# Kernel tuning notes

Hardware: AMD Instinct MI355X
Metric: run time of the kernel (lower is better)

The kernel has to match this reference:

```python
import jax, jax.numpy as jnp
import numpy as np

KERNEL_MUL = 2.0
KERNEL_NUM = 5
THRESH = 0.5            # cfg.FIXED_CONFIDENCE_THRESHOLD
LAMBDA = 1.0            # cfg.ECDA_CLASS_ATTENTION_LAMBDA
GAMMA = 0.1             # cfg.ECDA_COMPACTNESS_WEIGHT_GAMMA
DELTA = 0.01            # cfg.ECDA_REPULSION_WEIGHT_DELTA
NUM_CLASSES = 8
N, D = 2048, 256


def _sqdist(a, b):
    # pairwise squared euclidean distances [Na, Nb]
    d2 = (jnp.sum(a * a, 1)[:, None] + jnp.sum(b * b, 1)[None, :]
          - 2.0 * (a @ b.T))
    return jnp.maximum(d2, 0.0)


def setup_inputs() -> dict:
    key = jax.random.key(0)
    ks = jax.random.split(key, 6)
    return {
        'clean_feats': jax.random.normal(ks[0], (N, D), dtype=jnp.float32),
        'noisy_feats': jax.random.normal(ks[1], (N, D), dtype=jnp.float32),
        'clean_labels': jax.random.randint(ks[2], (N,), 0, NUM_CLASSES),
        'noisy_labels': jax.random.randint(ks[3], (N,), 0, NUM_CLASSES),
        'noisy_mask': jax.random.uniform(ks[4], (N,), dtype=jnp.float32),
        'noisy_scores': jax.random.uniform(ks[5], (N,), dtype=jnp.float32),
        'class_weights_wce': jax.random.uniform(jax.random.fold_in(key, 7), (NUM_CLASSES,), dtype=jnp.float32),
    }


def reference(clean_feats, noisy_feats, clean_labels, noisy_labels,
              noisy_mask, noisy_scores, class_weights_wce):
    C = class_weights_wce.shape[0]
    mask_n = noisy_mask > THRESH                       # float mask -> bool (cfg threshold)

    # full pairwise squared-distance matrices, reused by every class
    D_cc = _sqdist(clean_feats, clean_feats)           # [Nc, Nc]
    D_nn = _sqdist(noisy_feats, noisy_feats)           # [Nn, Nn]
    D_cn = _sqdist(clean_feats, noisy_feats)           # [Nc, Nn]

    classes = jnp.arange(C)
    Ms = (clean_labels[None, :] == classes[:, None]).astype(jnp.float32)   # [C, Nc]
    Mn = ((noisy_labels[None, :] == classes[:, None]) & mask_n[None, :]).astype(jnp.float32)  # [C, Nn]

    # noisy centroids + repulsion over valid classes (torch.pdist mean, negated)
    counts_n = Mn.sum(1)
    centroids = (Mn @ noisy_feats) / jnp.maximum(counts_n, 1.0)[:, None]
    valid = counts_n > 0
    Dcen = jnp.sqrt(jnp.maximum(_sqdist(centroids, centroids), 1e-12))
    pair = jnp.triu(jnp.ones((C, C), bool), 1) & valid[:, None] & valid[None, :]
    npairs = pair.sum().astype(jnp.float32)
    repulsion = jnp.where(valid.sum() > 1,
                          -jnp.sum(jnp.where(pair, Dcen, 0.0)) / jnp.maximum(npairs, 1.0),
                          0.0)

    attn = jnp.exp(LAMBDA * (class_weights_wce.mean() - class_weights_wce))
    half = KERNEL_MUL ** (KERNEL_NUM // 2)

    total = jnp.float32(0.0)
    for c in range(C):
        ms = Ms[c]                                     # clean weights (ones, masked)
        mn = Mn[c]
        n_s, n_t = ms.sum(), mn.sum()
        n = n_s + n_t
        # bandwidth from subset L2 sum (detached, as in .data)
        sumL2 = ms @ (D_cc @ ms) + mn @ (D_nn @ mn) + 2.0 * (ms @ (D_cn @ mn))
        sumL2 = jax.lax.stop_gradient(sumL2)
        bw0 = sumL2 / jnp.maximum(n * n - n, 1.0) / half
        wn = noisy_scores * mn                          # masked noisy weights
        ss = tt = st = jnp.float32(0.0)
        for k in range(KERNEL_NUM):
            bw = bw0 * (KERNEL_MUL ** k) + 1e-8
            ss = ss + ms @ (jnp.exp(-D_cc / bw) @ ms)
            tt = tt + wn @ (jnp.exp(-D_nn / bw) @ wn)
            st = st + ms @ (jnp.exp(-D_cn / bw) @ wn)
        sw = wn.sum()
        term_ss = ss / (n_s * n_s + 1e-8)
        term_tt = tt / (sw * sw + 1e-8)
        term_st = st / (n_s * sw + 1e-8)
        mmd = term_ss + term_tt - 2.0 * term_st
        compact = jnp.sum(mn * jnp.sum((noisy_feats - centroids[c]) ** 2, 1)) / jnp.maximum(n_t, 1.0)
        loss_c = mmd + GAMMA * compact + DELTA * repulsion
        total = total + jnp.where((n_s >= 2) & (n_t >= 2), attn[c] * loss_c, 0.0)
    return total
```

## Files before the change

kernel.cpp:

```cpp
#include <hip/hip_runtime.h>
#include <math.h>


static constexpr int NC = 8;
static constexpr int NN = 2048;
static constexpr int DD = 256;

static constexpr int OFF_CNT_S = 0;
static constexpr int OFF_CNT_T = 64;
static constexpr int OFF_SW    = 128;
static constexpr int OFF_COEF  = 192;
static constexpr int OFF_CCOMP = 256;
static constexpr int OFF_SQSP  = 1024;
static constexpr int OFF_SQTP  = 1536;
static constexpr int OFF_HDR   = 2048;
static constexpr int OFF_VSP   = 4096;
static constexpr int OFF_VTP   = 135168;
static constexpr int OFF_VS    = 266240;
static constexpr int OFF_VT    = 274432;
static constexpr int OFF_QBFS  = 282624;
static constexpr int OFF_QBFT  = 348160;
static constexpr int OFF_WTP   = 413696;
static constexpr size_t OFF_PKS = 479232;
static constexpr size_t OFF_PKT = 8867840;

typedef __attribute__((ext_vector_type(8))) short bf16x8;
typedef __attribute__((ext_vector_type(4))) float f32x4;

__device__ inline float wred64(float v) {
  for (int o = 32; o > 0; o >>= 1) v += __shfl_xor(v, o, 64);
  return v;
}
__device__ inline float brs256(float v, float* sh4) {
  for (int o = 32; o > 0; o >>= 1) v += __shfl_xor(v, o, 64);
  int w = threadIdx.x >> 6, ln = threadIdx.x & 63;
  __syncthreads();
  if (ln == 0) sh4[w] = v;
  __syncthreads();
  float r = 0.f;
  if (threadIdx.x == 0) r = sh4[0] + sh4[1] + sh4[2] + sh4[3];
  return r;
}

__global__ __launch_bounds__(256) void ecda_pack(
    const float* __restrict__ cfeat, const float* __restrict__ nfeat,
    const int* __restrict__ clab, const int* __restrict__ nlab,
    const float* __restrict__ nmask, const float* __restrict__ nscore,
    char* __restrict__ ws, float* __restrict__ out) {
  __shared__ int   ls_idx[NN];
  __shared__ float ls_wt[NN];
  __shared__ int   ls_cntw[4];
  __shared__ float ls_mom[4][256];
  __shared__ float ls_sq[4];
  __shared__ float sh4[4];
  int tid = threadIdx.x, bx = blockIdx.x;
  int wv = tid >> 6, lane = tid & 63;
  int typ = bx >> 7, c = (bx >> 4) & 7, chunk = bx & 15;

  if (bx == 0 && tid == 0) out[0] = 0.f;

  const int* labs = typ ? nlab : clab;
  const float* feats = typ ? nfeat : cfeat;

  int rb = wv * 512;
  int lv[8]; float mv[8], sv[8];
#pragma unroll
  for (int it = 0; it < 8; ++it) {
    int i = rb + it * 64 + lane;
    lv[it] = labs[i];
    if (typ) { mv[it] = nmask[i]; sv[it] = nscore[i]; }
  }
  unsigned long long msks[8];
  int cntw = 0;
#pragma unroll
  for (int it = 0; it < 8; ++it) {
    bool m = (lv[it] == c) && (!typ || mv[it] > 0.5f);
    msks[it] = __ballot(m);
    cntw += __popcll(msks[it]);
  }
  if (lane == 0) ls_cntw[wv] = cntw;
  __syncthreads();
  int base = 0;
  for (int w2 = 0; w2 < wv; ++w2) base += ls_cntw[w2];
#pragma unroll
  for (int it = 0; it < 8; ++it) {
    bool m = (msks[it] >> lane) & 1ull;
    int pos = __popcll(msks[it] & ((1ull << lane) - 1ull));
    if (m) {
      ls_idx[base + pos] = rb + it * 64 + lane;
      ls_wt[base + pos] = typ ? sv[it] : 1.f;
    }
    base += __popcll(msks[it]);
  }
  __syncthreads();
  int count = ls_cntw[0] + ls_cntw[1] + ls_cntw[2] + ls_cntw[3];

  if (chunk == 0) {
    if (tid == 0) (typ ? (int*)(ws + OFF_CNT_T) : (int*)(ws + OFF_CNT_S))[c] = count;
    if (typ) {
      float s = 0.f;
      for (int i = tid; i < count; i += 256) s += ls_wt[i];
      s = brs256(s, sh4);
      if (tid == 0) ((float*)(ws + OFF_SW))[c] = s;
    }
  }

  unsigned short* pk = (unsigned short*)(ws + (typ ? OFF_PKT : OFF_PKS)) + (size_t)c * NN * DD;
  float* qarr = (float*)(ws + (typ ? OFF_QBFT : OFF_QBFS)) + c * NN;
  float* wtp  = (float*)(ws + OFF_WTP) + c * NN;
  float vax = 0.f, vay = 0.f, vaz = 0.f, vaw = 0.f, qlane = 0.f;
  int mstart = chunk * 4 + wv;
  for (int m0 = mstart; m0 < count; m0 += 256) {
    int mm[4]; bool act[4]; float4 v[4];
#pragma unroll
    for (int b = 0; b < 4; ++b) {
      int m = m0 + b * 64;
      act[b] = (m < count);
      mm[b] = act[b] ? m : m0;
    }
#pragma unroll
    for (int b = 0; b < 4; ++b) {
      int idx = ls_idx[mm[b]];
      v[b] = *(const float4*)&feats[(size_t)idx * DD + lane * 4];
    }
#pragma unroll
    for (int b = 0; b < 4; ++b) {
      unsigned ux = __float_as_uint(v[b].x); ux = (ux + 0x7fffu + ((ux >> 16) & 1u)) & 0xffff0000u;
      unsigned uy = __float_as_uint(v[b].y); uy = (uy + 0x7fffu + ((uy >> 16) & 1u)) & 0xffff0000u;
      unsigned uz = __float_as_uint(v[b].z); uz = (uz + 0x7fffu + ((uz >> 16) & 1u)) & 0xffff0000u;
      unsigned uw = __float_as_uint(v[b].w); uw = (uw + 0x7fffu + ((uw >> 16) & 1u)) & 0xffff0000u;
      float rx = __uint_as_float(ux), ry = __uint_as_float(uy);
      float rz = __uint_as_float(uz), rw = __uint_as_float(uw);
      float rq = wred64(rx * rx + ry * ry + rz * rz + rw * rw);
      if (act[b]) {
        vax += v[b].x; vay += v[b].y; vaz += v[b].z; vaw += v[b].w;
        qlane += v[b].x * v[b].x + v[b].y * v[b].y + v[b].z * v[b].z + v[b].w * v[b].w;
        ushort4 b4;
        b4.x = (unsigned short)(ux >> 16); b4.y = (unsigned short)(uy >> 16);
        b4.z = (unsigned short)(uz >> 16); b4.w = (unsigned short)(uw >> 16);
        *(ushort4*)&pk[(size_t)mm[b] * DD + lane * 4] = b4;
        if (lane == 0) {
          qarr[mm[b]] = rq;
          if (typ) wtp[mm[b]] = ls_wt[mm[b]];
        }
      }
    }
  }
  float sqa = wred64(qlane);
  ls_mom[wv][lane * 4 + 0] = vax; ls_mom[wv][lane * 4 + 1] = vay;
  ls_mom[wv][lane * 4 + 2] = vaz; ls_mom[wv][lane * 4 + 3] = vaw;
  if (lane == 0) ls_sq[wv] = sqa;
  __syncthreads();
  float s = ls_mom[0][tid] + ls_mom[1][tid] + ls_mom[2][tid] + ls_mom[3][tid];
  float* vp = (float*)(ws + (typ ? OFF_VTP : OFF_VSP)) + (c * 16 + chunk) * 256;
  vp[tid] = s;
  if (tid == 0)
    ((float*)(ws + (typ ? OFF_SQTP : OFF_SQSP)))[c * 16 + chunk] =
        ls_sq[0] + ls_sq[1] + ls_sq[2] + ls_sq[3];
}

__global__ __launch_bounds__(256) void ecda_scalars(
    const float* __restrict__ cw, char* __restrict__ ws) {
  __shared__ float sh4[4];
  int c = blockIdx.x, tid = threadIdx.x;
  const float* vsp = (const float*)(ws + OFF_VSP);
  const float* vtp = (const float*)(ws + OFF_VTP);
  float vsd = 0.f, vtd = 0.f;
#pragma unroll
  for (int ch = 0; ch < 16; ++ch) {
    vsd += vsp[(c * 16 + ch) * 256 + tid];
    vtd += vtp[(c * 16 + ch) * 256 + tid];
  }
  ((float*)(ws + OFF_VS))[c * 256 + tid] = vsd;
  ((float*)(ws + OFF_VT))[c * 256 + tid] = vtd;
  float dss = brs256(vsd * vsd, sh4);
  float dtt = brs256(vtd * vtd, sh4);
  float dst = brs256(vsd * vtd, sh4);
  if (tid == 0) {
    const float* sqsp = (const float*)(ws + OFF_SQSP);
    const float* sqtp = (const float*)(ws + OFF_SQTP);
    float sqs = 0.f, sqt = 0.f;
    for (int ch = 0; ch < 16; ++ch) { sqs += sqsp[c * 16 + ch]; sqt += sqtp[c * 16 + ch]; }
    int nsi = ((const int*)(ws + OFF_CNT_S))[c];
    int nti = ((const int*)(ws + OFF_CNT_T))[c];
    float ns = (float)nsi, nt = (float)nti, n = ns + nt;
    float sumL2 = 2.f * ns * sqs - 2.f * dss
                + 2.f * nt * sqt - 2.f * dtt
                + 2.f * (nt * sqs + ns * sqt - 2.f * dst);
    float bw0 = sumL2 / fmaxf(n * n - n, 1.f) * 0.25f;
    float ib[5];
    float mul = 1.f;
    for (int k = 0; k < 5; ++k) { ib[k] = 1.f / (bw0 * mul + 1e-8f); mul *= 2.f; }
    float meanw = 0.f;
    for (int c2 = 0; c2 < NC; ++c2) meanw += cw[c2];
    meanw *= (1.f / NC);
    float attn = expf(meanw - cw[c]);
    float coef = (nsi >= 2 && nti >= 2) ? attn : 0.f;
    float swc = ((const float*)(ws + OFF_SW))[c];
    float scc = coef / (ns * ns + 1e-8f);
    float snn = coef / (swc * swc + 1e-8f);
    float scn = -2.f * coef / (ns * swc + 1e-8f);
    float* hdr = (float*)(ws + OFF_HDR);
    for (int ty = 0; ty < 3; ++ty) {
      float* h = hdr + (ty * 8 + c) * 8;
      int na = (ty == 1) ? nti : nsi;
      int nb = (ty == 0) ? nsi : nti;
      h[0] = __int_as_float(na);
      h[1] = __int_as_float(nb);
      h[2] = (ty == 0) ? scc : (ty == 1) ? snn : scn;
      h[3] = ib[0]; h[4] = ib[1]; h[5] = ib[2]; h[6] = ib[3]; h[7] = ib[4];
    }
    float mx = fmaxf(nt, 1.f);
    float compact = (sqt - 2.f * dtt / mx + nt * dtt / (mx * mx)) / mx;
    ((float*)(ws + OFF_COEF))[c] = coef;
    ((float*)(ws + OFF_CCOMP))[c] = coef * 0.1f * compact;
  }
}

__global__ __launch_bounds__(256) void ecda_pairs(
    const float* __restrict__ cw, char* __restrict__ ws,
    float* __restrict__ out) {
  __shared__ float shred[4];
  __shared__ float dcen[28];
  int tid = threadIdx.x, bx = blockIdx.x;
  int wv = tid >> 6, lane = tid & 63;

  if (bx == 384) {
    const int* cnt_t = (const int*)(ws + OFF_CNT_T);
    const float* vt = (const float*)(ws + OFF_VT);
    for (int t = wv; t < 28; t += 4) {
      int a = 0, r = t;
      while (r >= 7 - a) { r -= 7 - a; ++a; }
      int b = a + 1 + r;
      float ima = 1.f / fmaxf((float)cnt_t[a], 1.f);
      float imb = 1.f / fmaxf((float)cnt_t[b], 1.f);
      float4 x = *(const float4*)&vt[a * DD + lane * 4];
      float4 y = *(const float4*)&vt[b * DD + lane * 4];
      float dx = x.x * ima - y.x * imb, dy = x.y * ima - y.y * imb;
      float dz = x.z * ima - y.z * imb, dw = x.w * ima - y.w * imb;
      float ssum = wred64(dx * dx + dy * dy + dz * dz + dw * dw);
      if (lane == 0) dcen[t] = sqrtf(fmaxf(ssum, 1e-12f));
    }
    __syncthreads();
    if (tid == 0) {
      int nvalid = 0;
      for (int c2 = 0; c2 < NC; ++c2) nvalid += (cnt_t[c2] > 0);
      float sumD = 0.f; int np = 0; int p = 0;
      for (int a = 0; a < NC; ++a)
        for (int b = a + 1; b < NC; ++b) {
          if (cnt_t[a] > 0 && cnt_t[b] > 0) { sumD += dcen[p]; ++np; }
          ++p;
        }
      float repl = (nvalid > 1) ? (-sumD / fmaxf((float)np, 1.f)) : 0.f;
      const float* coefA = (const float*)(ws + OFF_COEF);
      const float* ccomp = (const float*)(ws + OFF_CCOMP);
      float base2 = 0.f, csum = 0.f;
      for (int c2 = 0; c2 < NC; ++c2) { base2 += ccomp[c2]; csum += coefA[c2]; }
      base2 += 0.01f * repl * csum;
      atomicAdd(out, base2);
    }
    return;
  }

  int par   = bx & 1;
  int rtile = (bx >> 1) & 7;
  int c     = (bx >> 4) & 7;
  int type  = bx >> 7;

  const f32x4* H = (const f32x4*)((const char*)ws + OFF_HDR) + (type * 8 + c) * 2;
  f32x4 h0 = H[0];
  int na = __float_as_int(h0[0]);
  int nb = __float_as_int(h0[1]);
  float scale = h0[2];
  int rbase = rtile * 32;
  if (scale == 0.f || rbase >= na || nb <= 0) return;
  int ct0 = (type <= 1) ? rtile : 0;
  int nbt = (nb + 31) >> 5;
  if (ct0 + par >= nbt) return;
  f32x4 h1 = H[1];
  float ib0 = h0[3], ib1 = h1[0], ib2 = h1[1], ib3 = h1[2], ib4 = h1[3];

  const unsigned short* pkS = (const unsigned short*)(ws + OFF_PKS) + (size_t)c * NN * DD;
  const unsigned short* pkT = (const unsigned short*)(ws + OFF_PKT) + (size_t)c * NN * DD;
  const float* qbS = (const float*)(ws + OFF_QBFS) + c * NN;
  const float* qbT = (const float*)(ws + OFF_QBFT) + c * NN;
  const float* wtp = (const float*)(ws + OFF_WTP) + c * NN;
  const unsigned short* pkA = (type == 1) ? pkT : pkS;
  const unsigned short* pkB = (type == 0) ? pkS : pkT;
  const float* qaB = (type == 1) ? qbT : qbS;
  const float* qbB = (type == 0) ? qbS : qbT;

  int sr = (wv >> 1) * 16, sc2 = (wv & 1) * 16;
  int posA = rbase + sr + (lane & 15);
  int pAc = posA < na ? posA : (na - 1);
  const unsigned short* rowA = pkA + (size_t)pAc * DD + (lane >> 4) * 8;
  bf16x8 afr[8];
#pragma unroll
  for (int ks = 0; ks < 8; ++ks) afr[ks] = *(const bf16x8*)(rowA + ks * 32);
  int rowbase = rbase + sr + ((lane >> 4) << 2);
  f32x4 qA4 = *(const f32x4*)&qaB[rowbase];
  f32x4 wA4 = {1.f, 1.f, 1.f, 1.f};
  if (type == 1) wA4 = *(const f32x4*)&wtp[rowbase];

  float lacc = 0.f;
  for (int ctile = ct0 + par; ctile < nbt; ctile += 2) {
    int cbase = ctile * 32;
    int posB = cbase + sc2 + (lane & 15);
    int pBc = posB < nb ? posB : (nb - 1);
    const unsigned short* rowB = pkB + (size_t)pBc * DD + (lane >> 4) * 8;
    f32x4 acc = {0.f, 0.f, 0.f, 0.f};
#pragma unroll
    for (int ks = 0; ks < 8; ++ks) {
      bf16x8 bf = *(const bf16x8*)(rowB + ks * 32);
      acc = __builtin_amdgcn_mfma_f32_16x16x32_bf16(afr[ks], bf, acc, 0, 0, 0);
    }
    bool jval = (posB < nb);
    float knj = qbB[pBc];
    float wj = (type == 0) ? 1.f : wtp[pBc];
    float factor = (type <= 1 && ctile > rtile) ? 2.f : 1.f;
    float partial = 0.f;
#pragma unroll
    for (int r = 0; r < 4; ++r) {
      int ip = rowbase + r;
      bool val = jval && (ip < na);
      float d2 = fmaxf(qA4[r] + knj - 2.f * acc[r], 0.f);
      float e = __expf(-d2 * ib0) + __expf(-d2 * ib1) + __expf(-d2 * ib2)
              + __expf(-d2 * ib3) + __expf(-d2 * ib4);
      float wgt = (type == 1) ? wA4[r] * wj : wj;
      partial += val ? wgt * e : 0.f;
    }
    lacc += factor * partial;
  }
  lacc = wred64(lacc);
  if (lane == 0) shred[wv] = lacc;
  __syncthreads();
  if (tid == 0) {
    float tot = shred[0] + shred[1] + shred[2] + shred[3];
    if (tot != 0.f) atomicAdd(out, scale * tot);
  }
}

extern "C" void kernel_launch(void* const* d_in, const int* in_sizes, int n_in,
                              void* d_out, int out_size, void* d_ws, size_t ws_size,
                              hipStream_t stream) {
  const float* cfeat  = (const float*)d_in[0];
  const float* nfeat  = (const float*)d_in[1];
  const int*   clab   = (const int*)d_in[2];
  const int*   nlab   = (const int*)d_in[3];
  const float* nmask  = (const float*)d_in[4];
  const float* nscore = (const float*)d_in[5];
  const float* cw     = (const float*)d_in[6];
  float* out = (float*)d_out;
  char* ws = (char*)d_ws;

  ecda_pack<<<256, 256, 0, stream>>>(cfeat, nfeat, clab, nlab, nmask, nscore,
                                     ws, out);
  ecda_scalars<<<8, 256, 0, stream>>>(cw, ws);
  ecda_pairs<<<385, 256, 0, stream>>>(cw, ws, out);
}
```

Measured before the change: 27.71 us.

## Fuse pack and scalar kernels into per-class stats kernel; split pair tiles 4-way

Merges the gather/pack kernel and the per-class scalar reduction kernel into one kernel with one 512-thread block per class. This removes the partial-sum workspace arrays and one launch. The pairs kernel now splits column tiles four ways instead of two, doubling its block count. The cost is that packing of all features now runs on only 8 blocks, which sharply reduces parallelism for the memory-bound gather.

```diff
diff --git a/kernel.cpp b/kernel.cpp
--- a/kernel.cpp
+++ b/kernel.cpp
@@ -8,15 +8,9 @@
 
 static constexpr int OFF_CNT_S = 0;
 static constexpr int OFF_CNT_T = 64;
-static constexpr int OFF_SW    = 128;
 static constexpr int OFF_COEF  = 192;
 static constexpr int OFF_CCOMP = 256;
-static constexpr int OFF_SQSP  = 1024;
-static constexpr int OFF_SQTP  = 1536;
 static constexpr int OFF_HDR   = 2048;
-static constexpr int OFF_VSP   = 4096;
-static constexpr int OFF_VTP   = 135168;
-static constexpr int OFF_VS    = 266240;
 static constexpr int OFF_VT    = 274432;
 static constexpr int OFF_QBFS  = 282624;
 static constexpr int OFF_QBFT  = 348160;
@@ -31,159 +25,150 @@
   for (int o = 32; o > 0; o >>= 1) v += __shfl_xor(v, o, 64);
   return v;
 }
-__device__ inline float brs256(float v, float* sh4) {
-  for (int o = 32; o > 0; o >>= 1) v += __shfl_xor(v, o, 64);
+__device__ inline float brs512(float v, float* sh8) {
+  v = wred64(v);
   int w = threadIdx.x >> 6, ln = threadIdx.x & 63;
   __syncthreads();
-  if (ln == 0) sh4[w] = v;
+  if (ln == 0) sh8[w] = v;
   __syncthreads();
   float r = 0.f;
-  if (threadIdx.x == 0) r = sh4[0] + sh4[1] + sh4[2] + sh4[3];
+  if (threadIdx.x == 0)
+    for (int i = 0; i < 8; ++i) r += sh8[i];
   return r;
 }
 
-__global__ __launch_bounds__(256) void ecda_pack(
+__global__ __launch_bounds__(512) void ecda_stats(
     const float* __restrict__ cfeat, const float* __restrict__ nfeat,
     const int* __restrict__ clab, const int* __restrict__ nlab,
     const float* __restrict__ nmask, const float* __restrict__ nscore,
-    char* __restrict__ ws, float* __restrict__ out) {
+    const float* __restrict__ cw, char* __restrict__ ws,
+    float* __restrict__ out) {
   __shared__ int   ls_idx[NN];
   __shared__ float ls_wt[NN];
-  __shared__ int   ls_cntw[4];
-  __shared__ float ls_mom[4][256];
-  __shared__ float ls_sq[4];
-  __shared__ float sh4[4];
-  int tid = threadIdx.x, bx = blockIdx.x;
-  int wv = tid >> 6, lane = tid & 63;
-  int typ = bx >> 7, c = (bx >> 4) & 7, chunk = bx & 15;
-
-  if (bx == 0 && tid == 0) out[0] = 0.f;
-
-  const int* labs = typ ? nlab : clab;
-  const float* feats = typ ? nfeat : cfeat;
-
-  int rb = wv * 512;
-  int lv[8]; float mv[8], sv[8];
-#pragma unroll
-  for (int it = 0; it < 8; ++it) {
-    int i = rb + it * 64 + lane;
-    lv[it] = labs[i];
-    if (typ) { mv[it] = nmask[i]; sv[it] = nscore[i]; }
-  }
-  unsigned long long msks[8];
-  int cntw = 0;
-#pragma unroll
-  for (int it = 0; it < 8; ++it) {
-    bool m = (lv[it] == c) && (!typ || mv[it] > 0.5f);
-    msks[it] = __ballot(m);
-    cntw += __popcll(msks[it]);
-  }
-  if (lane == 0) ls_cntw[wv] = cntw;
-  __syncthreads();
-  int base = 0;
-  for (int w2 = 0; w2 < wv; ++w2) base += ls_cntw[w2];
-#pragma unroll
-  for (int it = 0; it < 8; ++it) {
-    bool m = (msks[it] >> lane) & 1ull;
-    int pos = __popcll(msks[it] & ((1ull << lane) - 1ull));
-    if (m) {
-      ls_idx[base + pos] = rb + it * 64 + lane;
-      ls_wt[base + pos] = typ ? sv[it] : 1.f;
-    }
-    base += __popcll(msks[it]);
-  }
-  __syncthreads();
-  int count = ls_cntw[0] + ls_cntw[1] + ls_cntw[2] + ls_cntw[3];
-
-  if (chunk == 0) {
-    if (tid == 0) (typ ? (int*)(ws + OFF_CNT_T) : (int*)(ws + OFF_CNT_S))[c] = count;
-    if (typ) {
-      float s = 0.f;
-      for (int i = tid; i < count; i += 256) s += ls_wt[i];
-      s = brs256(s, sh4);
-      if (tid == 0) ((float*)(ws + OFF_SW))[c] = s;
-    }
-  }
-
-  unsigned short* pk = (unsigned short*)(ws + (typ ? OFF_PKT : OFF_PKS)) + (size_t)c * NN * DD;
-  float* qarr = (float*)(ws + (typ ? OFF_QBFT : OFF_QBFS)) + c * NN;
-  float* wtp  = (float*)(ws + OFF_WTP) + c * NN;
-  float vax = 0.f, vay = 0.f, vaz = 0.f, vaw = 0.f, qlane = 0.f;
-  int mstart = chunk * 4 + wv;
-  for (int m0 = mstart; m0 < count; m0 += 256) {
-    int mm[4]; bool act[4]; float4 v[4];
-#pragma unroll
-    for (int b = 0; b < 4; ++b) {
-      int m = m0 + b * 64;
-      act[b] = (m < count);
-      mm[b] = act[b] ? m : m0;
-    }
-#pragma unroll
-    for (int b = 0; b < 4; ++b) {
-      int idx = ls_idx[mm[b]];
-      v[b] = *(const float4*)&feats[(size_t)idx * DD + lane * 4];
-    }
-#pragma unroll
-    for (int b = 0; b < 4; ++b) {
-      unsigned ux = __float_as_uint(v[b].x); ux = (ux + 0x7fffu + ((ux >> 16) & 1u)) & 0xffff0000u;
-      unsigned uy = __float_as_uint(v[b].y); uy = (uy + 0x7fffu + ((uy >> 16) & 1u)) & 0xffff0000u;
-      unsigned uz = __float_as_uint(v[b].z); uz = (uz + 0x7fffu + ((uz >> 16) & 1u)) & 0xffff0000u;
-      unsigned uw = __float_as_uint(v[b].w); uw = (uw + 0x7fffu + ((uw >> 16) & 1u)) & 0xffff0000u;
-      float rx = __uint_as_float(ux), ry = __uint_as_float(uy);
-      float rz = __uint_as_float(uz), rw = __uint_as_float(uw);
-      float rq = wred64(rx * rx + ry * ry + rz * rz + rw * rw);
-      if (act[b]) {
-        vax += v[b].x; vay += v[b].y; vaz += v[b].z; vaw += v[b].w;
-        qlane += v[b].x * v[b].x + v[b].y * v[b].y + v[b].z * v[b].z + v[b].w * v[b].w;
-        ushort4 b4;
-        b4.x = (unsigned short)(ux >> 16); b4.y = (unsigned short)(uy >> 16);
-        b4.z = (unsigned short)(uz >> 16); b4.w = (unsigned short)(uw >> 16);
-        *(ushort4*)&pk[(size_t)mm[b] * DD + lane * 4] = b4;
-        if (lane == 0) {
-          qarr[mm[b]] = rq;
-          if (typ) wtp[mm[b]] = ls_wt[mm[b]];
+  __shared__ int   ls_cntw[8];
+  __shared__ float ls_mom[8][256];
+  __shared__ float ls_s1[8];
+  __shared__ float ls_s2[8];
+  __shared__ float vsr[256], vtr[256];
+  __shared__ float sh8[8];
+  __shared__ float s_sc[3];
+  __shared__ int   s_cnt[2];
+  int tid = threadIdx.x, c = blockIdx.x;
+  int w = tid >> 6, lane = tid & 63;
+  if (c == 0 && tid == 0) out[0] = 0.f;
+
+  for (int typ = 0; typ < 2; ++typ) {
+    const int* labs = typ ? nlab : clab;
+    const float* feats = typ ? nfeat : cfeat;
+    int rb = w * 256;
+    int lv[4]; float mv[4], sv[4];
+#pragma unroll
+    for (int it = 0; it < 4; ++it) {
+      int i = rb + it * 64 + lane;
+      lv[it] = labs[i];
+      if (typ) { mv[it] = nmask[i]; sv[it] = nscore[i]; }
+    }
+    unsigned long long msks[4]; int cntw = 0;
+#pragma unroll
+    for (int it = 0; it < 4; ++it) {
+      bool m = (lv[it] == c) && (!typ || mv[it] > 0.5f);
+      msks[it] = __ballot(m);
+      cntw += __popcll(msks[it]);
+    }
+    __syncthreads();
+    if (lane == 0) ls_cntw[w] = cntw;
+    __syncthreads();
+    int base = 0, count = 0;
+    for (int w2 = 0; w2 < 8; ++w2) {
+      if (w2 < w) base += ls_cntw[w2];
+      count += ls_cntw[w2];
+    }
+    int myend = base + cntw;
+    {
+      int b2 = base;
+#pragma unroll
+      for (int it = 0; it < 4; ++it) {
+        bool m = (msks[it] >> lane) & 1ull;
+        int pos = __popcll(msks[it] & ((1ull << lane) - 1ull));
+        if (m) {
+          ls_idx[b2 + pos] = rb + it * 64 + lane;
+          if (typ) ls_wt[b2 + pos] = sv[it];
+        }
+        b2 += __popcll(msks[it]);
+      }
+    }
+    __syncthreads();
+
+    unsigned short* pk = (unsigned short*)(ws + (typ ? OFF_PKT : OFF_PKS)) + (size_t)c * NN * DD;
+    float* qarr = (float*)(ws + (typ ? OFF_QBFT : OFF_QBFS)) + c * NN;
+    float* wtp  = (float*)(ws + OFF_WTP) + c * NN;
+    float vax = 0.f, vay = 0.f, vaz = 0.f, vaw = 0.f, qlane = 0.f, swv = 0.f;
+    for (int p0 = base; p0 < myend; p0 += 8) {
+      float4 v[8]; int mm[8]; bool act[8];
+#pragma unroll
+      for (int b = 0; b < 8; ++b) {
+        int p = p0 + b;
+        act[b] = (p < myend);
+        mm[b] = act[b] ? p : base;
+      }
+#pragma unroll
+      for (int b = 0; b < 8; ++b)
+        v[b] = *(const float4*)&feats[(size_t)ls_idx[mm[b]] * DD + lane * 4];
+#pragma unroll
+      for (int b = 0; b < 8; ++b) {
+        unsigned ux = __float_as_uint(v[b].x); ux = (ux + 0x7fffu + ((ux >> 16) & 1u)) & 0xffff0000u;
+        unsigned uy = __float_as_uint(v[b].y); uy = (uy + 0x7fffu + ((uy >> 16) & 1u)) & 0xffff0000u;
+        unsigned uz = __float_as_uint(v[b].z); uz = (uz + 0x7fffu + ((uz >> 16) & 1u)) & 0xffff0000u;
+        unsigned uw = __float_as_uint(v[b].w); uw = (uw + 0x7fffu + ((uw >> 16) & 1u)) & 0xffff0000u;
+        float rx = __uint_as_float(ux), ry = __uint_as_float(uy);
+        float rz = __uint_as_float(uz), rw = __uint_as_float(uw);
+        float rq = wred64(rx * rx + ry * ry + rz * rz + rw * rw);
+        if (act[b]) {
+          vax += v[b].x; vay += v[b].y; vaz += v[b].z; vaw += v[b].w;
+          qlane += v[b].x * v[b].x + v[b].y * v[b].y + v[b].z * v[b].z + v[b].w * v[b].w;
+          ushort4 b4;
+          b4.x = (unsigned short)(ux >> 16); b4.y = (unsigned short)(uy >> 16);
+          b4.z = (unsigned short)(uz >> 16); b4.w = (unsigned short)(uw >> 16);
+          *(ushort4*)&pk[(size_t)mm[b] * DD + lane * 4] = b4;
+          if (lane == 0) {
+            qarr[mm[b]] = rq;
+            if (typ) { float wv2 = ls_wt[mm[b]]; wtp[mm[b]] = wv2; swv += wv2; }
+          }
         }
       }
     }
-  }
-  float sqa = wred64(qlane);
-  ls_mom[wv][lane * 4 + 0] = vax; ls_mom[wv][lane * 4 + 1] = vay;
-  ls_mom[wv][lane * 4 + 2] = vaz; ls_mom[wv][lane * 4 + 3] = vaw;
-  if (lane == 0) ls_sq[wv] = sqa;
-  __syncthreads();
-  float s = ls_mom[0][tid] + ls_mom[1][tid] + ls_mom[2][tid] + ls_mom[3][tid];
-  float* vp = (float*)(ws + (typ ? OFF_VTP : OFF_VSP)) + (c * 16 + chunk) * 256;
-  vp[tid] = s;
-  if (tid == 0)
-    ((float*)(ws + (typ ? OFF_SQTP : OFF_SQSP)))[c * 16 + chunk] =
-        ls_sq[0] + ls_sq[1] + ls_sq[2] + ls_sq[3];
-}
-
-__global__ __launch_bounds__(256) void ecda_scalars(
-    const float* __restrict__ cw, char* __restrict__ ws) {
-  __shared__ float sh4[4];
-  int c = blockIdx.x, tid = threadIdx.x;
-  const float* vsp = (const float*)(ws + OFF_VSP);
-  const float* vtp = (const float*)(ws + OFF_VTP);
-  float vsd = 0.f, vtd = 0.f;
-#pragma unroll
-  for (int ch = 0; ch < 16; ++ch) {
-    vsd += vsp[(c * 16 + ch) * 256 + tid];
-    vtd += vtp[(c * 16 + ch) * 256 + tid];
-  }
-  ((float*)(ws + OFF_VS))[c * 256 + tid] = vsd;
-  ((float*)(ws + OFF_VT))[c * 256 + tid] = vtd;
-  float dss = brs256(vsd * vsd, sh4);
-  float dtt = brs256(vtd * vtd, sh4);
-  float dst = brs256(vsd * vtd, sh4);
+    ls_mom[w][lane * 4 + 0] = vax; ls_mom[w][lane * 4 + 1] = vay;
+    ls_mom[w][lane * 4 + 2] = vaz; ls_mom[w][lane * 4 + 3] = vaw;
+    float sq_w = wred64(qlane);
+    float sw_w = wred64(swv);
+    if (lane == 0) { ls_s1[w] = sq_w; ls_s2[w] = sw_w; }
+    __syncthreads();
+    if (tid < 256) {
+      float s = 0.f;
+#pragma unroll
+      for (int w2 = 0; w2 < 8; ++w2) s += ls_mom[w2][tid];
+      if (typ) { vtr[tid] = s; ((float*)(ws + OFF_VT))[c * 256 + tid] = s; }
+      else vsr[tid] = s;
+    }
+    if (tid == 0) {
+      float s1 = 0.f, s2 = 0.f;
+      for (int w2 = 0; w2 < 8; ++w2) { s1 += ls_s1[w2]; s2 += ls_s2[w2]; }
+      s_sc[typ] = s1;
+      if (typ) s_sc[2] = s2;
+      s_cnt[typ] = count;
+    }
+    __syncthreads();
+  }
+
+  float a = (tid < 256) ? vsr[tid] : 0.f;
+  float b = (tid < 256) ? vtr[tid] : 0.f;
+  float dss = brs512(a * a, sh8);
+  float dtt = brs512(b * b, sh8);
+  float dst = brs512(a * b, sh8);
   if (tid == 0) {
-    const float* sqsp = (const float*)(ws + OFF_SQSP);
-    const float* sqtp = (const float*)(ws + OFF_SQTP);
-    float sqs = 0.f, sqt = 0.f;
-    for (int ch = 0; ch < 16; ++ch) { sqs += sqsp[c * 16 + ch]; sqt += sqtp[c * 16 + ch]; }
-    int nsi = ((const int*)(ws + OFF_CNT_S))[c];
-    int nti = ((const int*)(ws + OFF_CNT_T))[c];
-    float ns = (float)nsi, nt = (float)nti, n = ns + nt;
+    int cnt0 = s_cnt[0], cnt1 = s_cnt[1];
+    float sqs = s_sc[0], sqt = s_sc[1], swc = s_sc[2];
+    float ns = (float)cnt0, nt = (float)cnt1, n = ns + nt;
     float sumL2 = 2.f * ns * sqs - 2.f * dss
                 + 2.f * nt * sqt - 2.f * dtt
                 + 2.f * (nt * sqs + ns * sqt - 2.f * dst);
@@ -195,16 +180,15 @@
     for (int c2 = 0; c2 < NC; ++c2) meanw += cw[c2];
     meanw *= (1.f / NC);
     float attn = expf(meanw - cw[c]);
-    float coef = (nsi >= 2 && nti >= 2) ? attn : 0.f;
-    float swc = ((const float*)(ws + OFF_SW))[c];
+    float coef = (cnt0 >= 2 && cnt1 >= 2) ? attn : 0.f;
     float scc = coef / (ns * ns + 1e-8f);
     float snn = coef / (swc * swc + 1e-8f);
     float scn = -2.f * coef / (ns * swc + 1e-8f);
     float* hdr = (float*)(ws + OFF_HDR);
     for (int ty = 0; ty < 3; ++ty) {
       float* h = hdr + (ty * 8 + c) * 8;
-      int na = (ty == 1) ? nti : nsi;
-      int nb = (ty == 0) ? nsi : nti;
+      int na = (ty == 1) ? cnt1 : cnt0;
+      int nb = (ty == 0) ? cnt0 : cnt1;
       h[0] = __int_as_float(na);
       h[1] = __int_as_float(nb);
       h[2] = (ty == 0) ? scc : (ty == 1) ? snn : scn;
@@ -214,18 +198,19 @@
     float compact = (sqt - 2.f * dtt / mx + nt * dtt / (mx * mx)) / mx;
     ((float*)(ws + OFF_COEF))[c] = coef;
     ((float*)(ws + OFF_CCOMP))[c] = coef * 0.1f * compact;
+    ((int*)(ws + OFF_CNT_S))[c] = cnt0;
+    ((int*)(ws + OFF_CNT_T))[c] = cnt1;
   }
 }
 
 __global__ __launch_bounds__(256) void ecda_pairs(
-    const float* __restrict__ cw, char* __restrict__ ws,
-    float* __restrict__ out) {
+    char* __restrict__ ws, float* __restrict__ out) {
   __shared__ float shred[4];
   __shared__ float dcen[28];
   int tid = threadIdx.x, bx = blockIdx.x;
   int wv = tid >> 6, lane = tid & 63;
 
-  if (bx == 384) {
+  if (bx == 768) {
     const int* cnt_t = (const int*)(ws + OFF_CNT_T);
     const float* vt = (const float*)(ws + OFF_VT);
     for (int t = wv; t < 28; t += 4) {
@@ -262,10 +247,10 @@
     return;
   }
 
-  int par   = bx & 1;
-  int rtile = (bx >> 1) & 7;
-  int c     = (bx >> 4) & 7;
-  int type  = bx >> 7;
+  int par   = bx & 3;
+  int rtile = (bx >> 2) & 7;
+  int c     = (bx >> 5) & 7;
+  int type  = bx >> 8;
 
   const f32x4* H = (const f32x4*)((const char*)ws + OFF_HDR) + (type * 8 + c) * 2;
   f32x4 h0 = H[0];
@@ -303,7 +288,7 @@
   if (type == 1) wA4 = *(const f32x4*)&wtp[rowbase];
 
   float lacc = 0.f;
-  for (int ctile = ct0 + par; ctile < nbt; ctile += 2) {
+  for (int ctile = ct0 + par; ctile < nbt; ctile += 4) {
     int cbase = ctile * 32;
     int posB = cbase + sc2 + (lane & 15);
     int pBc = posB < nb ? posB : (nb - 1);
@@ -353,8 +338,7 @@
   float* out = (float*)d_out;
   char* ws = (char*)d_ws;
 
-  ecda_pack<<<256, 256, 0, stream>>>(cfeat, nfeat, clab, nlab, nmask, nscore,
-                                     ws, out);
-  ecda_scalars<<<8, 256, 0, stream>>>(cw, ws);
-  ecda_pairs<<<385, 256, 0, stream>>>(cw, ws, out);
-}
+  ecda_stats<<<8, 512, 0, stream>>>(cfeat, nfeat, clab, nlab, nmask, nscore,
+                                    cw, ws, out);
+  ecda_pairs<<<769, 256, 0, stream>>>(ws, out);
+}
```

Result: slower. 49.35 us (+78.1%).

## Double grid parallelism in pack and pairs kernels, prefetch next B tile

Applied to the files above, without the earlier changes.

Splits the pack kernel across 32 chunks per class instead of 16 and the pairs kernel across 4 column-parity lanes instead of 2, doubling block counts to fill more CUs. The partial-sum workspace regions are enlarged and the scalars kernel now reduces 32 partials. The pairs inner loop software-pipelines the B-operand loads, fetching the next column tile's bf16 fragments while the current tile's MFMA and exp work runs. This raises register pressure and adds reduction work in exchange for more parallelism and hidden load latency.

```diff
diff --git a/kernel.cpp b/kernel.cpp
--- a/kernel.cpp
+++ b/kernel.cpp
@@ -12,17 +12,17 @@
 static constexpr int OFF_COEF  = 192;
 static constexpr int OFF_CCOMP = 256;
 static constexpr int OFF_SQSP  = 1024;
-static constexpr int OFF_SQTP  = 1536;
-static constexpr int OFF_HDR   = 2048;
+static constexpr int OFF_SQTP  = 2048;
+static constexpr int OFF_HDR   = 3072;
 static constexpr int OFF_VSP   = 4096;
-static constexpr int OFF_VTP   = 135168;
-static constexpr int OFF_VS    = 266240;
-static constexpr int OFF_VT    = 274432;
-static constexpr int OFF_QBFS  = 282624;
-static constexpr int OFF_QBFT  = 348160;
-static constexpr int OFF_WTP   = 413696;
-static constexpr size_t OFF_PKS = 479232;
-static constexpr size_t OFF_PKT = 8867840;
+static constexpr int OFF_VTP   = 266240;
+static constexpr int OFF_VS    = 528384;
+static constexpr int OFF_VT    = 536576;
+static constexpr int OFF_QBFS  = 544768;
+static constexpr int OFF_QBFT  = 610304;
+static constexpr int OFF_WTP   = 675840;
+static constexpr size_t OFF_PKS = 741376;
+static constexpr size_t OFF_PKT = 9129984;
 
 typedef __attribute__((ext_vector_type(8))) short bf16x8;
 typedef __attribute__((ext_vector_type(4))) float f32x4;
@@ -55,7 +55,7 @@
   __shared__ float sh4[4];
   int tid = threadIdx.x, bx = blockIdx.x;
   int wv = tid >> 6, lane = tid & 63;
-  int typ = bx >> 7, c = (bx >> 4) & 7, chunk = bx & 15;
+  int typ = bx >> 8, c = (bx >> 5) & 7, chunk = bx & 31;
 
   if (bx == 0 && tid == 0) out[0] = 0.f;
 
@@ -110,11 +110,11 @@
   float* wtp  = (float*)(ws + OFF_WTP) + c * NN;
   float vax = 0.f, vay = 0.f, vaz = 0.f, vaw = 0.f, qlane = 0.f;
   int mstart = chunk * 4 + wv;
-  for (int m0 = mstart; m0 < count; m0 += 256) {
+  for (int m0 = mstart; m0 < count; m0 += 512) {
     int mm[4]; bool act[4]; float4 v[4];
 #pragma unroll
     for (int b = 0; b < 4; ++b) {
-      int m = m0 + b * 64;
+      int m = m0 + b * 128;
       act[b] = (m < count);
       mm[b] = act[b] ? m : m0;
     }
@@ -152,10 +152,10 @@
   if (lane == 0) ls_sq[wv] = sqa;
   __syncthreads();
   float s = ls_mom[0][tid] + ls_mom[1][tid] + ls_mom[2][tid] + ls_mom[3][tid];
-  float* vp = (float*)(ws + (typ ? OFF_VTP : OFF_VSP)) + (c * 16 + chunk) * 256;
+  float* vp = (float*)(ws + (typ ? OFF_VTP : OFF_VSP)) + (c * 32 + chunk) * 256;
   vp[tid] = s;
   if (tid == 0)
-    ((float*)(ws + (typ ? OFF_SQTP : OFF_SQSP)))[c * 16 + chunk] =
+    ((float*)(ws + (typ ? OFF_SQTP : OFF_SQSP)))[c * 32 + chunk] =
         ls_sq[0] + ls_sq[1] + ls_sq[2] + ls_sq[3];
 }
 
@@ -167,9 +167,9 @@
   const float* vtp = (const float*)(ws + OFF_VTP);
   float vsd = 0.f, vtd = 0.f;
 #pragma unroll
-  for (int ch = 0; ch < 16; ++ch) {
-    vsd += vsp[(c * 16 + ch) * 256 + tid];
-    vtd += vtp[(c * 16 + ch) * 256 + tid];
+  for (int ch = 0; ch < 32; ++ch) {
+    vsd += vsp[(c * 32 + ch) * 256 + tid];
+    vtd += vtp[(c * 32 + ch) * 256 + tid];
   }
   ((float*)(ws + OFF_VS))[c * 256 + tid] = vsd;
   ((float*)(ws + OFF_VT))[c * 256 + tid] = vtd;
@@ -180,7 +180,7 @@
     const float* sqsp = (const float*)(ws + OFF_SQSP);
     const float* sqtp = (const float*)(ws + OFF_SQTP);
     float sqs = 0.f, sqt = 0.f;
-    for (int ch = 0; ch < 16; ++ch) { sqs += sqsp[c * 16 + ch]; sqt += sqtp[c * 16 + ch]; }
+    for (int ch = 0; ch < 32; ++ch) { sqs += sqsp[c * 32 + ch]; sqt += sqtp[c * 32 + ch]; }
     int nsi = ((const int*)(ws + OFF_CNT_S))[c];
     int nti = ((const int*)(ws + OFF_CNT_T))[c];
     float ns = (float)nsi, nt = (float)nti, n = ns + nt;
@@ -218,14 +218,13 @@
 }
 
 __global__ __launch_bounds__(256) void ecda_pairs(
-    const float* __restrict__ cw, char* __restrict__ ws,
-    float* __restrict__ out) {
+    char* __restrict__ ws, float* __restrict__ out) {
   __shared__ float shred[4];
   __shared__ float dcen[28];
   int tid = threadIdx.x, bx = blockIdx.x;
   int wv = tid >> 6, lane = tid & 63;
 
-  if (bx == 384) {
+  if (bx == 768) {
     const int* cnt_t = (const int*)(ws + OFF_CNT_T);
     const float* vt = (const float*)(ws + OFF_VT);
     for (int t = wv; t < 28; t += 4) {
@@ -262,10 +261,10 @@
     return;
   }
 
-  int par   = bx & 1;
-  int rtile = (bx >> 1) & 7;
-  int c     = (bx >> 4) & 7;
-  int type  = bx >> 7;
+  int par   = bx & 3;
+  int rtile = (bx >> 2) & 7;
+  int c     = (bx >> 5) & 7;
+  int type  = bx >> 8;
 
   const f32x4* H = (const f32x4*)((const char*)ws + OFF_HDR) + (type * 8 + c) * 2;
   f32x4 h0 = H[0];
@@ -302,21 +301,41 @@
   f32x4 wA4 = {1.f, 1.f, 1.f, 1.f};
   if (type == 1) wA4 = *(const f32x4*)&wtp[rowbase];
 
-  float lacc = 0.f;
-  for (int ctile = ct0 + par; ctile < nbt; ctile += 2) {
-    int cbase = ctile * 32;
-    int posB = cbase + sc2 + (lane & 15);
+  int ctile = ct0 + par;
+  bf16x8 bfr[8];
+  float knj, wj;
+  bool jval;
+  {
+    int posB = ctile * 32 + sc2 + (lane & 15);
     int pBc = posB < nb ? posB : (nb - 1);
     const unsigned short* rowB = pkB + (size_t)pBc * DD + (lane >> 4) * 8;
+#pragma unroll
+    for (int ks = 0; ks < 8; ++ks) bfr[ks] = *(const bf16x8*)(rowB + ks * 32);
+    knj = qbB[pBc];
+    wj = (type == 0) ? 1.f : wtp[pBc];
+    jval = (posB < nb);
+  }
+  float lacc = 0.f;
+  while (true) {
+    int nct = ctile + 4;
+    bf16x8 bfn[8];
+    float knjN = 0.f, wjN = 1.f;
+    bool jvalN = false;
+    bool have_next = (nct < nbt);
+    if (have_next) {
+      int posB = nct * 32 + sc2 + (lane & 15);
+      int pBc = posB < nb ? posB : (nb - 1);
+      const unsigned short* rowB = pkB + (size_t)pBc * DD + (lane >> 4) * 8;
+#pragma unroll
+      for (int ks = 0; ks < 8; ++ks) bfn[ks] = *(const bf16x8*)(rowB + ks * 32);
+      knjN = qbB[pBc];
+      wjN = (type == 0) ? 1.f : wtp[pBc];
+      jvalN = (posB < nb);
+    }
     f32x4 acc = {0.f, 0.f, 0.f, 0.f};
 #pragma unroll
-    for (int ks = 0; ks < 8; ++ks) {
-      bf16x8 bf = *(const bf16x8*)(rowB + ks * 32);
-      acc = __builtin_amdgcn_mfma_f32_16x16x32_bf16(afr[ks], bf, acc, 0, 0, 0);
-    }
-    bool jval = (posB < nb);
-    float knj = qbB[pBc];
-    float wj = (type == 0) ? 1.f : wtp[pBc];
+    for (int ks = 0; ks < 8; ++ks)
+      acc = __builtin_amdgcn_mfma_f32_16x16x32_bf16(afr[ks], bfr[ks], acc, 0, 0, 0);
     float factor = (type <= 1 && ctile > rtile) ? 2.f : 1.f;
     float partial = 0.f;
 #pragma unroll
@@ -330,6 +349,11 @@
       partial += val ? wgt * e : 0.f;
     }
     lacc += factor * partial;
+    if (!have_next) break;
+    ctile = nct;
+#pragma unroll
+    for (int ks = 0; ks < 8; ++ks) bfr[ks] = bfn[ks];
+    knj = knjN; wj = wjN; jval = jvalN;
   }
   lacc = wred64(lacc);
   if (lane == 0) shred[wv] = lacc;
@@ -353,8 +377,8 @@
   float* out = (float*)d_out;
   char* ws = (char*)d_ws;
 
-  ecda_pack<<<256, 256, 0, stream>>>(cfeat, nfeat, clab, nlab, nmask, nscore,
+  ecda_pack<<<512, 256, 0, stream>>>(cfeat, nfeat, clab, nlab, nmask, nscore,
                                      ws, out);
   ecda_scalars<<<8, 256, 0, stream>>>(cw, ws);
-  ecda_pairs<<<385, 256, 0, stream>>>(cw, ws, out);
-}
+  ecda_pairs<<<769, 256, 0, stream>>>(ws, out);
+}
```

Measured after the change: 30.35 us. 9.6% more time.
